# Performance work log

Hardware: AMD Instinct MI355X
Metric: run time of the kernel (lower is better)

Reference implementation:

```python
import jax, jax.numpy as jnp
import numpy as np

B, GRID, D, NF, NC = 4096, 8, 64, 256, 10
N = GRID * GRID          # num_nodes = grid_size**2
LN_EPS = 1e-5            # torch LayerNorm default eps


def _grid_mask():
    m = np.zeros((N, N), np.float32)
    for i in range(N):
        r, c = divmod(i, GRID)
        if r > 0: m[i, i - GRID] = 1
        if r < GRID - 1: m[i, i + GRID] = 1
        if c > 0: m[i, i - 1] = 1
        if c < GRID - 1: m[i, i + 1] = 1
    return jnp.asarray(m)

MASK = _grid_mask()  # static 4-neighbor grid adjacency mask [N,N]


def _ln(x, g, b):
    mu = x.mean(-1, keepdims=True)
    v = ((x - mu) ** 2).mean(-1, keepdims=True)  # biased var, like torch LayerNorm
    return (x - mu) / jnp.sqrt(v + LN_EPS) * g + b


def _regulator(x, h_pre, w_norm, p):
    # HomeostaticRegulator.forward (eval mode: baselines fixed at 0.5 / 1.0)
    var = jnp.var(x, axis=1, ddof=1, keepdims=True)            # torch.var default unbiased=True
    natural_stress = jnp.abs(var - 0.5)
    xs = jnp.sort(x, axis=1)
    smoothness = jnp.abs(xs[:, 1:] - xs[:, :-1]).mean(1, keepdims=True)
    adversarial_stress = jnp.abs(smoothness - 1.0)
    excitation = jnp.abs(h_pre).mean(1, keepdims=True)
    fatigue = jnp.broadcast_to(jnp.reshape(w_norm, (1, 1)), (x.shape[0], 1))
    gradient_proxy = jnp.sqrt((h_pre ** 2).mean(1, keepdims=True))
    s = jnp.concatenate([natural_stress, adversarial_stress, excitation, fatigue, gradient_proxy], axis=1)
    h = jnp.tanh(_ln(s @ p[0].T + p[1], p[2], p[3]))
    h = jnp.tanh(_ln(h @ p[4].T + p[5], p[6], p[7]))
    return jax.nn.sigmoid(h @ p[8].T + p[9])  # [B,3] = metabolism, sensitivity, gate


def _cell(x, W_slow, W_fast, ln_g, ln_b, cp):
    # HomeoContinuumCell.forward, eval mode (no Hebbian buffer update)
    h_raw = jax.lax.stop_gradient(x @ W_slow.T)                 # computed under torch.no_grad
    w_norm = jax.lax.stop_gradient(jnp.sqrt((W_slow ** 2).sum()))
    ctl = _regulator(x, h_raw, w_norm, cp)
    beta = 0.5 + ctl[:, 1:2] * 2.0
    gate = ctl[:, 2:3]
    comb = x @ W_slow.T + (x @ W_fast.T) * gate
    act = comb * jax.nn.sigmoid(beta * comb)
    return _ln(act, ln_g, ln_b)


def _forward(x, W_embed, b_embed, adj_weights, W_slow, W_fast, ln_g, ln_b, W_read, b_read, tp, cp):
    e = x @ W_embed.T + b_embed                                 # [B, N*D]
    e3 = e.reshape(B, N, D)
    # HomeoTopology.get_adjacency with homeostasis (all under no_grad in torch)
    ts = jax.lax.stop_gradient(e.reshape(1, -1))                # flatten whole batch state
    wn = jax.lax.stop_gradient(jnp.sqrt((adj_weights ** 2).sum()))
    ctl = jax.lax.stop_gradient(_regulator(ts, ts, wn, tp))
    ap = ctl[:, 0].mean()                                       # plasticity(=1.0) * mean metabolism
    adj = jax.nn.sigmoid(adj_weights * ap) * MASK
    adj = adj / jnp.clip(adj.sum(1, keepdims=True), 1e-6, None)
    m = jnp.einsum('nm,bmd->bnd', adj, e3)                      # grid message passing
    proc = _cell(m.reshape(B * N, D), W_slow, W_fast, ln_g, ln_b, cp)
    return proc.reshape(B, N * D) @ W_read.T + b_read           # logits [B, NC]


def _reg_params(key, scale=0.2):
    ks = jax.random.split(key, 3)
    return (jax.random.normal(ks[0], (16, 5)) * scale, jnp.zeros(16), jnp.ones(16), jnp.zeros(16),
            jax.random.normal(ks[1], (8, 16)) * scale, jnp.zeros(8), jnp.ones(8), jnp.zeros(8),
            jax.random.normal(ks[2], (3, 8)) * scale, jnp.zeros(3))


def setup_inputs() -> dict:
    key = jax.random.key(0)
    ks = jax.random.split(key, 9)
    inp = {
        'x': jax.random.normal(ks[0], (B, NF)),
        'W_embed': jax.random.normal(ks[1], (N * D, NF)) * (1.0 / np.sqrt(NF)),
        'b_embed': jnp.zeros(N * D),
        'adj_weights': jax.random.normal(ks[2], (N, N)) * 0.1,
        'W_slow': jax.random.normal(ks[3], (D, D)) * (1.4 / np.sqrt(D)),
        'W_fast': jax.random.normal(ks[4], (D, D)) * 0.05,
        'ln_g': jnp.ones(D), 'ln_b': jnp.zeros(D),
        'W_read': jax.random.normal(ks[5], (NC, N * D)) * (1.0 / np.sqrt(N * D)),
        'b_read': jnp.zeros(NC),
    }
    names = ['W1', 'b1', 'g1', 'bb1', 'W2', 'b2', 'g2', 'bb2', 'W3', 'b3']
    for pre, k in (('t', ks[6]), ('c', ks[7])):
        for n, v in zip(names, _reg_params(k)):
            inp[pre + '_' + n] = v
    return inp


def reference(x, W_embed, b_embed, adj_weights, W_slow, W_fast, ln_g, ln_b, W_read, b_read,
              t_W1, t_b1, t_g1, t_bb1, t_W2, t_b2, t_g2, t_bb2, t_W3, t_b3,
              c_W1, c_b1, c_g1, c_bb1, c_W2, c_b2, c_g2, c_bb2, c_W3, c_b3):
    tp = (t_W1, t_b1, t_g1, t_bb1, t_W2, t_b2, t_g2, t_bb2, t_W3, t_b3)
    cp = (c_W1, c_b1, c_g1, c_bb1, c_W2, c_b2, c_g2, c_bb2, c_W3, c_b3)
    return _forward(x, W_embed, b_embed, adj_weights, W_slow, W_fast, ln_g, ln_b, W_read, b_read, tp, cp)
```

## Files before the change

kernel.cpp:

```cpp
#include <hip/hip_runtime.h>

typedef unsigned short u16;
typedef unsigned int   u32;
typedef float f32x4 __attribute__((ext_vector_type(4)));
typedef int   i32x4 __attribute__((ext_vector_type(4)));
typedef int   i32x2 __attribute__((ext_vector_type(2)));
typedef short s8v   __attribute__((ext_vector_type(8)));

__device__ inline u16 f2bf(float f) {
  u32 u = __float_as_uint(f);
  return (u16)((u + 0x7FFFu + ((u >> 16) & 1u)) >> 16);
}
__device__ inline float bf2f(u16 h) { return __uint_as_float(((u32)h) << 16); }

__device__ inline u32 fkey(float f) {
  u32 u = __float_as_uint(f);
  return (u & 0x80000000u) ? ~u : (u | 0x80000000u);
}
__device__ inline float unkey(u32 k) {
  u32 u = (k & 0x80000000u) ? (k & 0x7FFFFFFFu) : ~k;
  return __uint_as_float(u);
}
__device__ inline float fast_tanh(float x) {
  float cx = fminf(fmaxf(x, -15.f), 15.f);
  float e = __expf(2.f * cx);
  return __fdividef(e - 1.f, e + 1.f);
}
__device__ inline float sigm(float x) { return __fdividef(1.f, 1.f + __expf(-x)); }

__device__ inline void gload_lds16(const u16* g, u16* l) {
  __builtin_amdgcn_global_load_lds((const __attribute__((address_space(1))) u32*)g,
                                   (__attribute__((address_space(3))) u32*)l, 16, 0, 0);
}

struct MlpP { const float *W1,*b1,*g1,*bb1,*W2,*b2,*g2,*bb2,*W3,*b3; };

__device__ inline void mlp_eval(const MlpP& p, const float* s, float* ctl) {
  float h1[16];
  float mu = 0.f;
  #pragma unroll
  for (int i = 0; i < 16; ++i) {
    float v = p.b1[i];
    #pragma unroll
    for (int k = 0; k < 5; ++k) v = fmaf(p.W1[i*5+k], s[k], v);
    h1[i] = v; mu += v;
  }
  mu *= (1.0f/16.0f);
  float vv = 0.f;
  #pragma unroll
  for (int i = 0; i < 16; ++i) { float d = h1[i]-mu; vv += d*d; }
  vv *= (1.0f/16.0f);
  float inv = 1.0f/sqrtf(vv + 1e-5f);
  #pragma unroll
  for (int i = 0; i < 16; ++i) h1[i] = fast_tanh((h1[i]-mu)*inv*p.g1[i] + p.bb1[i]);
  float h2[8];
  mu = 0.f;
  #pragma unroll
  for (int o = 0; o < 8; ++o) {
    float v = p.b2[o];
    #pragma unroll
    for (int i = 0; i < 16; ++i) v = fmaf(p.W2[o*16+i], h1[i], v);
    h2[o] = v; mu += v;
  }
  mu *= 0.125f;
  vv = 0.f;
  #pragma unroll
  for (int o = 0; o < 8; ++o) { float d = h2[o]-mu; vv += d*d; }
  vv *= 0.125f;
  inv = 1.0f/sqrtf(vv + 1e-5f);
  #pragma unroll
  for (int o = 0; o < 8; ++o) h2[o] = fast_tanh((h2[o]-mu)*inv*p.g2[o] + p.bb2[o]);
  #pragma unroll
  for (int c = 0; c < 3; ++c) {
    float v = p.b3[c];
    #pragma unroll
    for (int o = 0; o < 8; ++o) v = fmaf(p.W3[c*8+o], h2[o], v);
    ctl[c] = sigm(v);
  }
}

__global__ __launch_bounds__(256) void k_pre(const float* __restrict__ x,
                                             const float* __restrict__ We,
                                             const float* __restrict__ Ws,
                                             const float* __restrict__ Wf,
                                             u16* __restrict__ Xb, u16* __restrict__ Wb,
                                             u16* __restrict__ WsB, u16* __restrict__ WfB,
                                             float* __restrict__ S) {
  const int bi = blockIdx.x, t = threadIdx.x;
  if (bi < 2048) {
    const float* src = (bi < 1024) ? x : We;
    u16* dst = (bi < 1024) ? Xb : Wb;
    int i = ((bi & 1023) * 256 + t) * 4;
    f32x4 v = *(const f32x4*)(src + i);
    u16 o[4] = { f2bf(v[0]), f2bf(v[1]), f2bf(v[2]), f2bf(v[3]) };
    *(u32*)(dst + i)     = ((u32)o[1] << 16) | o[0];
    *(u32*)(dst + i + 2) = ((u32)o[3] << 16) | o[2];
  } else {
    #pragma unroll
    for (int m = 0; m < 2; ++m) {
      const float* src = m ? Wf : Ws;
      u16* dst = m ? WfB : WsB;
      int base = t * 16;
      u16 o[16];
      #pragma unroll
      for (int r = 0; r < 4; ++r) {
        f32x4 v = *(const f32x4*)(src + base + r*4);
        o[r*4+0]=f2bf(v[0]); o[r*4+1]=f2bf(v[1]); o[r*4+2]=f2bf(v[2]); o[r*4+3]=f2bf(v[3]);
      }
      #pragma unroll
      for (int r = 0; r < 8; ++r)
        *(u32*)(dst + base + r*2) = ((u32)o[r*2+1] << 16) | o[r*2];
    }
    if (t < 3) S[t] = 0.f;
    if (t == 3) ((u32*)S)[3] = 0xFFFFFFFFu;
    if (t == 4) ((u32*)S)[4] = 0u;
  }
}

__global__ __launch_bounds__(256) void k_gemm(const u16* __restrict__ Xb,
                                              const u16* __restrict__ Wb,
                                              const float* __restrict__ bias,
                                              u16* __restrict__ E,
                                              float* __restrict__ S) {
  __shared__ __align__(16) u16 As[128*64];
  __shared__ __align__(16) u16 Bs[128*64];
  const int t = threadIdx.x;
  const int wv = t >> 6, lane = t & 63;
  const int wr = wv >> 1, wc = wv & 1;
  const int i0 = blockIdx.y * 128, j0 = blockIdx.x * 128;
  const int rr = lane & 15, q = lane >> 4;
  const int lrow = lane >> 3, lcol = (lane & 7) * 8;
  f32x4 acc[4][4] = {};
  for (int k0 = 0; k0 < 256; k0 += 64) {
    #pragma unroll
    for (int r = 0; r < 4; ++r) {
      const int row = (r*4 + wv)*8 + lrow;
      gload_lds16(Xb + (size_t)(i0 + row)*256 + k0 + lcol, &As[(r*4 + wv)*512]);
      gload_lds16(Wb + (size_t)(j0 + row)*256 + k0 + lcol, &Bs[(r*4 + wv)*512]);
    }
    __syncthreads();
    #pragma unroll
    for (int ks = 0; ks < 2; ++ks) {
      s8v a[4], b[4];
      #pragma unroll
      for (int m = 0; m < 4; ++m) a[m] = *(const s8v*)&As[(wr*64 + m*16 + rr)*64 + ks*32 + q*8];
      #pragma unroll
      for (int n = 0; n < 4; ++n) b[n] = *(const s8v*)&Bs[(wc*64 + n*16 + rr)*64 + ks*32 + q*8];
      #pragma unroll
      for (int m = 0; m < 4; ++m)
        #pragma unroll
        for (int n = 0; n < 4; ++n)
          acc[m][n] = __builtin_amdgcn_mfma_f32_16x16x32_bf16(a[m], b[n], acc[m][n], 0, 0, 0);
    }
    __syncthreads();
  }
  float s = 0.f, ss = 0.f, sa = 0.f, mnv = 1e30f, mxv = -1e30f;
  #pragma unroll
  for (int n = 0; n < 4; ++n) {
    const int col = j0 + wc*64 + n*16 + rr;
    const float bv = bias[col];
    #pragma unroll
    for (int m = 0; m < 4; ++m) {
      const int rowb = i0 + wr*64 + m*16 + q*4;
      #pragma unroll
      for (int r = 0; r < 4; ++r) {
        float v = acc[m][n][r] + bv;
        E[(size_t)(rowb + r)*4096 + col] = f2bf(v);
        s += v; ss = fmaf(v, v, ss); sa += fabsf(v);
        mnv = fminf(mnv, v); mxv = fmaxf(mxv, v);
      }
    }
  }
  #pragma unroll
  for (int off = 32; off; off >>= 1) {
    s += __shfl_xor(s, off); ss += __shfl_xor(ss, off); sa += __shfl_xor(sa, off);
    mnv = fminf(mnv, __shfl_xor(mnv, off));
    mxv = fmaxf(mxv, __shfl_xor(mxv, off));
  }
  __shared__ float red5[4][5];
  if (lane == 0) { red5[wv][0]=s; red5[wv][1]=ss; red5[wv][2]=sa; red5[wv][3]=mnv; red5[wv][4]=mxv; }
  __syncthreads();
  if (t == 0) {
    float S0 = red5[0][0]+red5[1][0]+red5[2][0]+red5[3][0];
    float S1 = red5[0][1]+red5[1][1]+red5[2][1]+red5[3][1];
    float S2 = red5[0][2]+red5[1][2]+red5[2][2]+red5[3][2];
    float Mn = fminf(fminf(red5[0][3],red5[1][3]), fminf(red5[2][3],red5[3][3]));
    float Mx = fmaxf(fmaxf(red5[0][4],red5[1][4]), fmaxf(red5[2][4],red5[3][4]));
    atomicAdd(&S[0], S0); atomicAdd(&S[1], S1); atomicAdd(&S[2], S2);
    atomicMin((u32*)S + 3, fkey(Mn));
    atomicMax((u32*)S + 4, fkey(Mx));
  }
}

__global__ __launch_bounds__(256) void k_prep(const float* __restrict__ adjw,
    const float* __restrict__ Wslow,
    const float* tW1, const float* tb1, const float* tg1, const float* tbb1,
    const float* tW2, const float* tb2, const float* tg2, const float* tbb2,
    const float* tW3, const float* tb3,
    float* __restrict__ S) {
  __shared__ float red[2][256];
  __shared__ float apL;
  const int t = threadIdx.x;
  float a = 0.f, w = 0.f;
  for (int i = t; i < 4096; i += 256) {
    float v = adjw[i]; a = fmaf(v, v, a);
    float u = Wslow[i]; w = fmaf(u, u, w);
  }
  red[0][t] = a; red[1][t] = w;
  __syncthreads();
  for (int sred = 128; sred > 0; sred >>= 1) {
    if (t < sred) { red[0][t] += red[0][t+sred]; red[1][t] += red[1][t+sred]; }
    __syncthreads();
  }
  if (t == 0) {
    float wn_t = sqrtf(red[0][0]);
    float wn_c = sqrtf(red[1][0]);
    S[7] = wn_c;
    const float n = 16777216.0f, n1 = 16777215.0f;
    float sum = S[0], sumsq = S[1], sumabs = S[2];
    float mean = sum / n;
    float var = (sumsq - sum*mean) / n1;
    float mn = unkey(((u32*)S)[3]);
    float mx = unkey(((u32*)S)[4]);
    float sfv[5];
    sfv[0] = fabsf(var - 0.5f);
    sfv[1] = fabsf((mx - mn)/n1 - 1.0f);
    sfv[2] = sumabs / n;
    sfv[3] = wn_t;
    sfv[4] = sqrtf(sumsq / n);
    MlpP p{tW1,tb1,tg1,tbb1,tW2,tb2,tg2,tbb2,tW3,tb3};
    float ctl[3];
    mlp_eval(p, sfv, ctl);
    apL = ctl[0];
    S[6] = ctl[0];
  }
  __syncthreads();
  if (t < 64) {
    const int rr = t >> 3, cc = t & 7;
    const float ap = apL;
    const int nb[4] = { rr>0 ? t-8 : -1, rr<7 ? t+8 : -1, cc>0 ? t-1 : -1, cc<7 ? t+1 : -1 };
    float w4[4]; float rs = 0.f;
    #pragma unroll
    for (int qq = 0; qq < 4; ++qq) {
      w4[qq] = (nb[qq] >= 0) ? sigm(adjw[t*64 + nb[qq]] * ap) : 0.0f;
      rs += w4[qq];
    }
    rs = fmaxf(rs, 1e-6f);
    #pragma unroll
    for (int qq = 0; qq < 4; ++qq) S[8 + t*4 + qq] = w4[qq] / rs;
  }
}

__global__ __launch_bounds__(256, 5) void k_cell(const u16* __restrict__ E,
    const u16* __restrict__ WsB, const u16* __restrict__ WfB,
    const float* __restrict__ lng, const float* __restrict__ lnb,
    const float* __restrict__ Wread, const float* __restrict__ bread,
    const float* __restrict__ S,
    const float* cW1, const float* cb1, const float* cg1, const float* cbb1,
    const float* cW2, const float* cb2, const float* cg2, const float* cbb2,
    const float* cW3, const float* cb3,
    float* __restrict__ out) {
  __shared__ __align__(16) u16 ebM[64][72];
  __shared__ __align__(16) u16 WsH[64][72];
  __shared__ __align__(16) u16 WfH[64][72];
  __shared__ __align__(16) float adjcL[256];
  __shared__ __align__(16) float prm[308];
  __shared__ __align__(16) float lngL[64], lnbL[64];
  __shared__ float wncL;
  float* const sfvL = (float*)&ebM[0][0];
  float* const bgL  = (float*)&ebM[0][0] + 320;
  float* const wavp = (float*)&ebM[0][0] + 448;

  const int t = threadIdx.x;
  const int wv = t >> 6, lane = t & 63;
  const int b = blockIdx.x;
  const u16* Eb = E + (size_t)b * 4096;

  {
    const int row = t >> 2, c16 = (t & 3) * 16;
    *(i32x4*)&ebM[row][c16]     = *(const i32x4*)(Eb  + row*64 + c16);
    *(i32x4*)&ebM[row][c16 + 8] = *(const i32x4*)(Eb  + row*64 + c16 + 8);
    *(i32x4*)&WsH[row][c16]     = *(const i32x4*)(WsB + row*64 + c16);
    *(i32x4*)&WsH[row][c16 + 8] = *(const i32x4*)(WsB + row*64 + c16 + 8);
    *(i32x4*)&WfH[row][c16]     = *(const i32x4*)(WfB + row*64 + c16);
    *(i32x4*)&WfH[row][c16 + 8] = *(const i32x4*)(WfB + row*64 + c16 + 8);
  }
  adjcL[t] = S[8 + t];
  for (int i = t; i < 80;  i += 256) prm[i] = cW1[i];
  if (t < 16) { prm[80+t]=cb1[t]; prm[96+t]=cg1[t]; prm[112+t]=cbb1[t]; }
  for (int i = t; i < 128; i += 256) prm[128+i] = cW2[i];
  if (t < 8)  { prm[256+t]=cb2[t]; prm[264+t]=cg2[t]; prm[272+t]=cbb2[t]; }
  if (t < 24) prm[280+t] = cW3[t];
  if (t < 3)  prm[304+t] = cb3[t];
  if (t < 64) { lngL[t] = lng[t]; lnbL[t] = lnb[t]; }
  if (t == 0) wncL = S[7];
  __syncthreads();

  float macc[16];
  {
    const int d = lane;
    #pragma unroll
    for (int i = 0; i < 16; ++i) {
      const int n = wv*16 + i;
      const int gr = n >> 3, gc = n & 7;
      const int nb0 = gr > 0 ? n - 8 : 0;
      const int nb1 = gr < 7 ? n + 8 : 0;
      const int nb2 = gc > 0 ? n - 1 : 0;
      const int nb3 = gc < 7 ? n + 1 : 0;
      macc[i] = adjcL[n*4+0]*bf2f(ebM[nb0][d]) + adjcL[n*4+1]*bf2f(ebM[nb1][d])
              + adjcL[n*4+2]*bf2f(ebM[nb2][d]) + adjcL[n*4+3]*bf2f(ebM[nb3][d]);
    }
  }
  __syncthreads();
  #pragma unroll
  for (int i = 0; i < 16; ++i) ebM[wv*16 + i][lane] = f2bf(macc[i]);
  __syncthreads();

  const int rr = lane & 15, q = lane >> 4;
  const int n = wv*16 + rr;
  s8v bm0 = *(const s8v*)&ebM[n][q*8];
  s8v bm1 = *(const s8v*)&ebM[n][32 + q*8];
  f32x4 hs[4], hf[4];
  #pragma unroll
  for (int jt = 0; jt < 4; ++jt) {
    const u16* wsr = &WsH[jt*16 + rr][0];
    const u16* wfr = &WfH[jt*16 + rr][0];
    s8v aw0 = *(const s8v*)(wsr + q*8), aw1 = *(const s8v*)(wsr + 32 + q*8);
    s8v af0 = *(const s8v*)(wfr + q*8), af1 = *(const s8v*)(wfr + 32 + q*8);
    f32x4 z = {0.f, 0.f, 0.f, 0.f};
    hs[jt] = __builtin_amdgcn_mfma_f32_16x16x32_bf16(aw0, bm0, z, 0, 0, 0);
    hs[jt] = __builtin_amdgcn_mfma_f32_16x16x32_bf16(aw1, bm1, hs[jt], 0, 0, 0);
    hf[jt] = __builtin_amdgcn_mfma_f32_16x16x32_bf16(af0, bm0, z, 0, 0, 0);
    hf[jt] = __builtin_amdgcn_mfma_f32_16x16x32_bf16(af1, bm1, hf[jt], 0, 0, 0);
  }

  float s1 = 0.f, s2 = 0.f, mnv = 1e30f, mxv = -1e30f;
  #pragma unroll
  for (int j = 0; j < 8; ++j) {
    float v0 = bf2f((u16)bm0[j]), v1 = bf2f((u16)bm1[j]);
    s1 += v0 + v1;
    s2 = fmaf(v0, v0, s2); s2 = fmaf(v1, v1, s2);
    mnv = fminf(mnv, fminf(v0, v1));
    mxv = fmaxf(mxv, fmaxf(v0, v1));
  }
  float sa = 0.f, sq = 0.f;
  #pragma unroll
  for (int jt = 0; jt < 4; ++jt)
    #pragma unroll
    for (int r = 0; r < 4; ++r) { float v = hs[jt][r]; sa += fabsf(v); sq = fmaf(v, v, sq); }
  #pragma unroll
  for (int off = 16; off <= 32; off <<= 1) {
    s1 += __shfl_xor(s1, off); s2 += __shfl_xor(s2, off);
    sa += __shfl_xor(sa, off); sq += __shfl_xor(sq, off);
    mnv = fminf(mnv, __shfl_xor(mnv, off));
    mxv = fmaxf(mxv, __shfl_xor(mxv, off));
  }
  if (q == 0) {
    float var = (s2 - s1*s1*(1.f/64.f)) * (1.f/63.f);
    sfvL[n*5+0] = fabsf(var - 0.5f);
    sfvL[n*5+1] = fabsf((mxv - mnv)*(1.f/63.f) - 1.f);
    sfvL[n*5+2] = sa * (1.f/64.f);
    sfvL[n*5+3] = wncL;
    sfvL[n*5+4] = sqrtf(sq * (1.f/64.f));
  }
  __syncthreads();

  if (t < 64) {
    float sfv[5];
    #pragma unroll
    for (int k = 0; k < 5; ++k) sfv[k] = sfvL[t*5+k];
    MlpP p{prm, prm+80, prm+96, prm+112, prm+128, prm+256, prm+264, prm+272, prm+280, prm+304};
    float ctl[3];
    mlp_eval(p, sfv, ctl);
    bgL[t*2+0] = 0.5f + 2.f*ctl[1];
    bgL[t*2+1] = ctl[2];
  }
  __syncthreads();

  const float beta = bgL[n*2+0], gate = bgL[n*2+1];
  float acts[4][4];
  float a1 = 0.f, a2 = 0.f;
  #pragma unroll
  for (int jt = 0; jt < 4; ++jt)
    #pragma unroll
    for (int r = 0; r < 4; ++r) {
      float comb = fmaf(hf[jt][r], gate, hs[jt][r]);
      float sv = comb * sigm(beta * comb);
      acts[jt][r] = sv;
      a1 += sv; a2 = fmaf(sv, sv, a2);
    }
  a1 += __shfl_xor(a1, 16); a2 += __shfl_xor(a2, 16);
  a1 += __shfl_xor(a1, 32); a2 += __shfl_xor(a2, 32);
  float mu = a1 * (1.f/64.f);
  float vvv = a2 * (1.f/64.f) - mu*mu;
  float inv = 1.f / sqrtf(vvv + 1e-5f);
  float racc[10];
  #pragma unroll
  for (int c = 0; c < 10; ++c) racc[c] = 0.f;
  #pragma unroll
  for (int jt = 0; jt < 4; ++jt) {
    f32x4 gv = *(const f32x4*)&lngL[jt*16 + q*4];
    f32x4 bv = *(const f32x4*)&lnbL[jt*16 + q*4];
    float pr[4];
    #pragma unroll
    for (int r = 0; r < 4; ++r) pr[r] = (acts[jt][r] - mu)*inv*gv[r] + bv[r];
    const float* wrb = Wread + n*64 + jt*16 + q*4;
    #pragma unroll
    for (int c = 0; c < 10; ++c) {
      f32x4 w = *(const f32x4*)(wrb + c*4096);
      racc[c] += pr[0]*w[0] + pr[1]*w[1] + pr[2]*w[2] + pr[3]*w[3];
    }
  }
  #pragma unroll
  for (int c = 0; c < 10; ++c) {
    float v = racc[c];
    #pragma unroll
    for (int off = 1; off < 64; off <<= 1) v += __shfl_xor(v, off);
    if (lane == 0) wavp[wv*10 + c] = v;
  }
  __syncthreads();
  if (t < 10) out[(size_t)b*10 + t] = bread[t] + wavp[0*10+t] + wavp[1*10+t] + wavp[2*10+t] + wavp[3*10+t];
}

extern "C" void kernel_launch(void* const* d_in, const int* in_sizes, int n_in,
                              void* d_out, int out_size, void* d_ws, size_t ws_size,
                              hipStream_t stream) {
  (void)in_sizes; (void)n_in; (void)out_size; (void)ws_size;
  const float* x       = (const float*)d_in[0];
  const float* W_embed = (const float*)d_in[1];
  const float* b_embed = (const float*)d_in[2];
  const float* adjw    = (const float*)d_in[3];
  const float* Wslow   = (const float*)d_in[4];
  const float* Wfast   = (const float*)d_in[5];
  const float* lng     = (const float*)d_in[6];
  const float* lnb     = (const float*)d_in[7];
  const float* Wread   = (const float*)d_in[8];
  const float* bread   = (const float*)d_in[9];
  float* out = (float*)d_out;

  char* ws = (char*)d_ws;
  u16*   Ebf  = (u16*)ws;
  u16*   Xbf  = (u16*)(ws + 33554432);
  u16*   Wbf  = (u16*)(ws + 35651584);
  float* S    = (float*)(ws + 37748736);
  u16*   WsBf = (u16*)(ws + 37752832);
  u16*   WfBf = (u16*)(ws + 37761024);

  hipLaunchKernelGGL(k_pre, dim3(2049), dim3(256), 0, stream,
                     x, W_embed, Wslow, Wfast, Xbf, Wbf, WsBf, WfBf, S);
  hipLaunchKernelGGL(k_gemm, dim3(32, 32), dim3(256), 0, stream, Xbf, Wbf, b_embed, Ebf, S);
  hipLaunchKernelGGL(k_prep, dim3(1), dim3(256), 0, stream, adjw, Wslow,
                     (const float*)d_in[10], (const float*)d_in[11], (const float*)d_in[12], (const float*)d_in[13],
                     (const float*)d_in[14], (const float*)d_in[15], (const float*)d_in[16], (const float*)d_in[17],
                     (const float*)d_in[18], (const float*)d_in[19], S);
  hipLaunchKernelGGL(k_cell, dim3(4096), dim3(256), 0, stream, Ebf, WsBf, WfBf, lng, lnb,
                     Wread, bread, S,
                     (const float*)d_in[20], (const float*)d_in[21], (const float*)d_in[22], (const float*)d_in[23],
                     (const float*)d_in[24], (const float*)d_in[25], (const float*)d_in[26], (const float*)d_in[27],
                     (const float*)d_in[28], (const float*)d_in[29], out);
}
```

Baseline: 367.6 us.

## Double-buffer GEMM LDS tiles, swizzle block order, repack cell scratch

The embedding GEMM now double-buffers its A/B tiles in LDS, prefetching the next K slice while MFMAs run on the current one. It also uses a 1D grid with an XCD-aware swizzle of tile indices to improve L2 locality. In the cell kernel, the per-node regulator scratch moves into the padding columns of the ebM tile and wavp gets its own array. The occupancy hint drops from 5 to 4 blocks. The GEMM loop still has a barrier per iteration and uses twice the LDS, which may lower occupancy.

```diff
diff --git a/kernel.cpp b/kernel.cpp
--- a/kernel.cpp
+++ b/kernel.cpp
@@ -122,30 +122,43 @@
                                               const float* __restrict__ bias,
                                               u16* __restrict__ E,
                                               float* __restrict__ S) {
-  __shared__ __align__(16) u16 As[128*64];
-  __shared__ __align__(16) u16 Bs[128*64];
+  __shared__ __align__(16) u16 As[2][8192];
+  __shared__ __align__(16) u16 Bs[2][8192];
   const int t = threadIdx.x;
   const int wv = t >> 6, lane = t & 63;
   const int wr = wv >> 1, wc = wv & 1;
-  const int i0 = blockIdx.y * 128, j0 = blockIdx.x * 128;
+  const int bid = blockIdx.x;
+  const int sw = (bid & 7) * 128 + (bid >> 3);
+  const int i0 = (sw >> 5) * 128, j0 = (sw & 31) * 128;
   const int rr = lane & 15, q = lane >> 4;
   const int lrow = lane >> 3, lcol = (lane & 7) * 8;
+
   f32x4 acc[4][4] = {};
-  for (int k0 = 0; k0 < 256; k0 += 64) {
-    #pragma unroll
-    for (int r = 0; r < 4; ++r) {
-      const int row = (r*4 + wv)*8 + lrow;
-      gload_lds16(Xb + (size_t)(i0 + row)*256 + k0 + lcol, &As[(r*4 + wv)*512]);
-      gload_lds16(Wb + (size_t)(j0 + row)*256 + k0 + lcol, &Bs[(r*4 + wv)*512]);
-    }
-    __syncthreads();
+  #pragma unroll
+  for (int r = 0; r < 4; ++r) {
+    const int row = (r*4 + wv)*8 + lrow;
+    gload_lds16(Xb + (size_t)(i0 + row)*256 + lcol, &As[0][(r*4 + wv)*512]);
+    gload_lds16(Wb + (size_t)(j0 + row)*256 + lcol, &Bs[0][(r*4 + wv)*512]);
+  }
+  __syncthreads();
+  for (int it = 0; it < 4; ++it) {
+    const int cur = it & 1;
+    if (it < 3) {
+      const int k0 = (it + 1) * 64;
+      #pragma unroll
+      for (int r = 0; r < 4; ++r) {
+        const int row = (r*4 + wv)*8 + lrow;
+        gload_lds16(Xb + (size_t)(i0 + row)*256 + k0 + lcol, &As[cur^1][(r*4 + wv)*512]);
+        gload_lds16(Wb + (size_t)(j0 + row)*256 + k0 + lcol, &Bs[cur^1][(r*4 + wv)*512]);
+      }
+    }
     #pragma unroll
     for (int ks = 0; ks < 2; ++ks) {
       s8v a[4], b[4];
       #pragma unroll
-      for (int m = 0; m < 4; ++m) a[m] = *(const s8v*)&As[(wr*64 + m*16 + rr)*64 + ks*32 + q*8];
-      #pragma unroll
-      for (int n = 0; n < 4; ++n) b[n] = *(const s8v*)&Bs[(wc*64 + n*16 + rr)*64 + ks*32 + q*8];
+      for (int m = 0; m < 4; ++m) a[m] = *(const s8v*)&As[cur][(wr*64 + m*16 + rr)*64 + ks*32 + q*8];
+      #pragma unroll
+      for (int n = 0; n < 4; ++n) b[n] = *(const s8v*)&Bs[cur][(wc*64 + n*16 + rr)*64 + ks*32 + q*8];
       #pragma unroll
       for (int m = 0; m < 4; ++m)
         #pragma unroll
@@ -251,7 +264,7 @@
   }
 }
 
-__global__ __launch_bounds__(256, 5) void k_cell(const u16* __restrict__ E,
+__global__ __launch_bounds__(256, 4) void k_cell(const u16* __restrict__ E,
     const u16* __restrict__ WsB, const u16* __restrict__ WfB,
     const float* __restrict__ lng, const float* __restrict__ lnb,
     const float* __restrict__ Wread, const float* __restrict__ bread,
@@ -266,10 +279,8 @@
   __shared__ __align__(16) float adjcL[256];
   __shared__ __align__(16) float prm[308];
   __shared__ __align__(16) float lngL[64], lnbL[64];
+  __shared__ float wavp[4][10];
   __shared__ float wncL;
-  float* const sfvL = (float*)&ebM[0][0];
-  float* const bgL  = (float*)&ebM[0][0] + 320;
-  float* const wavp = (float*)&ebM[0][0] + 448;
 
   const int t = threadIdx.x;
   const int wv = t >> 6, lane = t & 63;
@@ -357,27 +368,28 @@
   }
   if (q == 0) {
     float var = (s2 - s1*s1*(1.f/64.f)) * (1.f/63.f);
-    sfvL[n*5+0] = fabsf(var - 0.5f);
-    sfvL[n*5+1] = fabsf((mxv - mnv)*(1.f/63.f) - 1.f);
-    sfvL[n*5+2] = sa * (1.f/64.f);
-    sfvL[n*5+3] = wncL;
-    sfvL[n*5+4] = sqrtf(sq * (1.f/64.f));
+    f32x4 sv = { fabsf(var - 0.5f),
+                 fabsf((mxv - mnv)*(1.f/63.f) - 1.f),
+                 sa * (1.f/64.f),
+                 sqrtf(sq * (1.f/64.f)) };
+    *(f32x4*)&ebM[n][64] = sv;
   }
   __syncthreads();
 
   if (t < 64) {
-    float sfv[5];
-    #pragma unroll
-    for (int k = 0; k < 5; ++k) sfv[k] = sfvL[t*5+k];
+    f32x4 sv = *(const f32x4*)&ebM[t][64];
+    float sfv[5] = { sv[0], sv[1], sv[2], wncL, sv[3] };
     MlpP p{prm, prm+80, prm+96, prm+112, prm+128, prm+256, prm+264, prm+272, prm+280, prm+304};
     float ctl[3];
     mlp_eval(p, sfv, ctl);
-    bgL[t*2+0] = 0.5f + 2.f*ctl[1];
-    bgL[t*2+1] = ctl[2];
-  }
-  __syncthreads();
-
-  const float beta = bgL[n*2+0], gate = bgL[n*2+1];
+    float* pad = (float*)&ebM[t][64];
+    pad[0] = 0.5f + 2.f*ctl[1];
+    pad[1] = ctl[2];
+  }
+  __syncthreads();
+
+  const float beta = ((const float*)&ebM[n][64])[0];
+  const float gate = ((const float*)&ebM[n][64])[1];
   float acts[4][4];
   float a1 = 0.f, a2 = 0.f;
   #pragma unroll
@@ -416,10 +428,10 @@
     float v = racc[c];
     #pragma unroll
     for (int off = 1; off < 64; off <<= 1) v += __shfl_xor(v, off);
-    if (lane == 0) wavp[wv*10 + c] = v;
-  }
-  __syncthreads();
-  if (t < 10) out[(size_t)b*10 + t] = bread[t] + wavp[0*10+t] + wavp[1*10+t] + wavp[2*10+t] + wavp[3*10+t];
+    if (lane == 0) wavp[wv][c] = v;
+  }
+  __syncthreads();
+  if (t < 10) out[(size_t)b*10 + t] = bread[t] + wavp[0][t] + wavp[1][t] + wavp[2][t] + wavp[3][t];
 }
 
 extern "C" void kernel_launch(void* const* d_in, const int* in_sizes, int n_in,
@@ -448,7 +460,7 @@
 
   hipLaunchKernelGGL(k_pre, dim3(2049), dim3(256), 0, stream,
                      x, W_embed, Wslow, Wfast, Xbf, Wbf, WsBf, WfBf, S);
-  hipLaunchKernelGGL(k_gemm, dim3(32, 32), dim3(256), 0, stream, Xbf, Wbf, b_embed, Ebf, S);
+  hipLaunchKernelGGL(k_gemm, dim3(1024), dim3(256), 0, stream, Xbf, Wbf, b_embed, Ebf, S);
   hipLaunchKernelGGL(k_prep, dim3(1), dim3(256), 0, stream, adjw, Wslow,
                      (const float*)d_in[10], (const float*)d_in[11], (const float*)d_in[12], (const float*)d_in[13],
                      (const float*)d_in[14], (const float*)d_in[15], (const float*)d_in[16], (const float*)d_in[17],
```

Result: faster. 338.8 us (-7.8%).
